# Optimization experiments

Measured on AMD Instinct MI355X. Metric: run time of the kernel, lower is better.

Reference implementation:

```python
import jax, jax.numpy as jnp
import numpy as np

N_NODES = 100000
N_EDGES = 1600000
NODE_DIM = 128
HIDDEN = 128
OUT_DIM = 128
N_GRAPHS = 64
LN_EPS = 1e-5


def setup_inputs() -> dict:
    key = jax.random.key(0)
    ks = jax.random.split(key, 14)

    def lin(k, fan_in, fan_out):
        bound = 1.0 / np.sqrt(fan_in)
        kw, kb = jax.random.split(k)
        W = jax.random.uniform(kw, (fan_in, fan_out), jnp.float32, -bound, bound)
        b = jax.random.uniform(kb, (fan_out,), jnp.float32, -bound, bound)
        return W, b

    node_features = jax.random.normal(ks[0], (N_NODES, NODE_DIM), jnp.float32)
    edge_index = jax.random.randint(ks[1], (2, N_EDGES), 0, N_NODES, jnp.int32)
    batch = jnp.sort(jax.random.randint(ks[2], (N_NODES,), 0, N_GRAPHS, jnp.int32))

    W1, b1 = lin(ks[3], NODE_DIM, HIDDEN)
    W2, b2 = lin(ks[4], HIDDEN, HIDDEN)
    W3, b3 = lin(ks[5], HIDDEN, OUT_DIM)
    Wm1, bm1 = lin(ks[6], OUT_DIM, HIDDEN)
    Wm2, bm2 = lin(ks[7], HIDDEN, OUT_DIM)
    ln_g = jnp.ones((OUT_DIM,), jnp.float32)
    ln_b = jnp.zeros((OUT_DIM,), jnp.float32)

    return dict(node_features=node_features, edge_index=edge_index, batch=batch,
                W1=W1, b1=b1, W2=W2, b2=b2, W3=W3, b3=b3,
                Wm1=Wm1, bm1=bm1, Wm2=Wm2, bm2=bm2, ln_g=ln_g, ln_b=ln_b)


def _gcn_precompute(edge_index, n_nodes):
    # Add self-loops; symmetric degree normalization (PyG GCNConv semantics).
    loops = jnp.arange(n_nodes, dtype=edge_index.dtype)
    src = jnp.concatenate([edge_index[0], loops])
    dst = jnp.concatenate([edge_index[1], loops])
    deg = jax.ops.segment_sum(jnp.ones_like(dst, jnp.float32), dst, num_segments=n_nodes)
    dinv = jax.lax.rsqrt(deg)  # deg >= 1 thanks to self-loops
    norm = dinv[src] * dinv[dst]  # [E + N]
    return src, dst, norm


def _gcn_layer(x, W, b, src, dst, norm, n_nodes):
    xw = x @ W                              # [N, F_out]
    msg = norm[:, None] * xw[src]           # [E+N, F_out] gather
    agg = jax.ops.segment_sum(msg, dst, num_segments=n_nodes)  # scatter-add
    return agg + b


def reference(node_features, edge_index, batch,
              W1, b1, W2, b2, W3, b3, Wm1, bm1, Wm2, bm2, ln_g, ln_b):
    n_nodes = node_features.shape[0]
    src, dst, norm = _gcn_precompute(edge_index, n_nodes)

    x = jax.nn.relu(_gcn_layer(node_features, W1, b1, src, dst, norm, n_nodes))
    x = jax.nn.relu(_gcn_layer(x, W2, b2, src, dst, norm, n_nodes))
    x = _gcn_layer(x, W3, b3, src, dst, norm, n_nodes)  # no relu on last layer

    # global mean pool per graph
    sums = jax.ops.segment_sum(x, batch, num_segments=N_GRAPHS)
    cnts = jax.ops.segment_sum(jnp.ones((n_nodes,), x.dtype), batch, num_segments=N_GRAPHS)
    g = sums / jnp.maximum(cnts, 1.0)[:, None]  # [G, OUT_DIM]

    # global reasoner MLP + LayerNorm
    h = jax.nn.relu(g @ Wm1 + bm1)
    y = h @ Wm2 + bm2
    mu = jnp.mean(y, axis=-1, keepdims=True)
    var = jnp.var(y, axis=-1, keepdims=True)
    y = (y - mu) * jax.lax.rsqrt(var + LN_EPS) * ln_g + ln_b
    return y
```

## Files before the change

kernel.cpp:

```cpp
#include <hip/hip_runtime.h>

#define FDIM 128
#define LN_EPS 1e-5f
#define NBKT_SHIFT 8
#define BKT_NODES 256
#define MAXBKT 512
#define CAP_SHIFT 13
#define BKT_CAP 8192

typedef short bf16x8 __attribute__((ext_vector_type(8)));
typedef float f32x4 __attribute__((ext_vector_type(4)));
typedef float f32x2 __attribute__((ext_vector_type(2)));
typedef ushort u16x8 __attribute__((ext_vector_type(8)));
typedef unsigned long long u64;
typedef long long i64;

static __device__ __forceinline__ ushort f2bf(float f) {
    union { float f; unsigned u; } v; v.f = f;
    unsigned r = v.u + 0x7FFFu + ((v.u >> 16) & 1u);
    return (ushort)(r >> 16);
}
static __device__ __forceinline__ float bf2f(ushort h) {
    union { unsigned u; float f; } v; v.u = ((unsigned)h) << 16;
    return v.f;
}
static __device__ __forceinline__ unsigned char f2fp8(float f) {
    return (unsigned char)__builtin_amdgcn_cvt_pk_fp8_f32(f, f, 0u, false);
}
static __device__ __forceinline__ float fp8tof(unsigned char b) {
    f32x2 p = __builtin_amdgcn_cvt_pk_f32_fp8((unsigned)b, false);
    return p[0];
}
static __device__ __forceinline__ void fp8x8_add(uint2 w, f32x2* acc) {
    acc[0] += __builtin_amdgcn_cvt_pk_f32_fp8(w.x, false);
    acc[1] += __builtin_amdgcn_cvt_pk_f32_fp8(w.x, true);
    acc[2] += __builtin_amdgcn_cvt_pk_f32_fp8(w.y, false);
    acc[3] += __builtin_amdgcn_cvt_pk_f32_fp8(w.y, true);
}

typedef __attribute__((address_space(3))) unsigned char lds_uchar;
typedef const __attribute__((address_space(1))) unsigned char glob_uchar;
static __device__ __forceinline__ void gload16(const unsigned char* g, unsigned char* l) {
    __builtin_amdgcn_global_load_lds((glob_uchar*)g, (lds_uchar*)l, 16, 0, 0);
}


__launch_bounds__(256)
__global__ void k_bkt_scatter(const int* __restrict__ src, const int* __restrict__ dst,
                              int* __restrict__ bcur, unsigned* __restrict__ bktA,
                              int E, int nbkt) {
    __shared__ int h[2][MAXBKT], lbase[2][MAXBKT], lcur[2][MAXBKT];
    const int t = threadIdx.x;
    const int half = t >> 7;
    for (int i = t; i < 2 * MAXBKT; i += 256) ((int*)h)[i] = 0;
    __syncthreads();
    const int E4 = E >> 2;
    const int4* s4p = (const int4*)src;
    const int4* d4p = (const int4*)dst;
    int4 sv[4], dv[4]; bool ok[4];
#pragma unroll
    for (int r = 0; r < 4; r++) {
        int i4 = blockIdx.x * 1024 + r * 256 + t;
        ok[r] = (i4 < E4);
        if (ok[r]) {
            sv[r] = s4p[i4]; dv[r] = d4p[i4];
            atomicAdd(&h[half][dv[r].x >> NBKT_SHIFT], 1);
            atomicAdd(&h[half][dv[r].y >> NBKT_SHIFT], 1);
            atomicAdd(&h[half][dv[r].z >> NBKT_SHIFT], 1);
            atomicAdd(&h[half][dv[r].w >> NBKT_SHIFT], 1);
        }
    }
    __syncthreads();
    for (int i = t; i < 2 * nbkt; i += 256) {
        const int hh = (i >= nbkt) ? 1 : 0;
        const int b = hh ? (i - nbkt) : i;
        const int c = h[hh][b];
        lbase[hh][b] = c ? ((b << CAP_SHIFT) + atomicAdd(&bcur[b], c)) : 0;
        lcur[hh][b] = 0;
    }
    __syncthreads();
#pragma unroll
    for (int r = 0; r < 4; r++) {
        if (!ok[r]) continue;
        int ss[4] = {sv[r].x, sv[r].y, sv[r].z, sv[r].w};
        int dd[4] = {dv[r].x, dv[r].y, dv[r].z, dv[r].w};
#pragma unroll
        for (int j = 0; j < 4; j++) {
            int b = dd[j] >> NBKT_SHIFT;
            int p = atomicAdd(&lcur[half][b], 1);
            bktA[(size_t)lbase[half][b] + p] =
                ((unsigned)ss[j] << NBKT_SHIFT) | (unsigned)(dd[j] & (BKT_NODES - 1));
        }
    }
}


__launch_bounds__(512)
__global__ void k_build(const unsigned* __restrict__ bktA, const int* __restrict__ bcur,
                        int2* __restrict__ rowinfo, float* __restrict__ dinv,
                        int* __restrict__ csr_src, int N) {
    __shared__ int sorted[BKT_CAP];
    __shared__ int cnt[BKT_NODES];
    __shared__ int cur[BKT_NODES];
    __shared__ int wpart[4], wbase[4];
    const int t = threadIdx.x;
    const int b = blockIdx.x;
    const int nb = b << NBKT_SHIFT;
    if (t < BKT_NODES) cnt[t] = 0;
    __syncthreads();
    const int beg = b << CAP_SHIFT;
    const int tot = bcur[b];
    for (int i = t; i < tot; i += 512)
        atomicAdd(&cnt[bktA[beg + i] & (BKT_NODES - 1)], 1);
    __syncthreads();
    const int lane = t & 63, wv = t >> 6;
    int my = 0, x = 0;
    if (t < BKT_NODES) {
        my = cnt[t];
        x = my;
#pragma unroll
        for (int off = 1; off < 64; off <<= 1) {
            int y = __shfl_up(x, off, 64);
            if (lane >= off) x += y;
        }
        if (lane == 63) wpart[wv] = x;
    }
    __syncthreads();
    if (t == 0) {
        int s = 0;
        for (int w = 0; w < 4; w++) { int tmp = wpart[w]; wbase[w] = s; s += tmp; }
    }
    __syncthreads();
    if (t < BKT_NODES) {
        const int incl = x + wbase[wv];
        const int rbeg = incl - my;
        cur[t] = rbeg;
        const int n = nb + t;
        if (n < N) {
            rowinfo[n] = make_int2(beg + rbeg, my);
            dinv[n] = rsqrtf((float)(my + 1));
        }
    }
    __syncthreads();
    for (int i = t; i < tot; i += 512) {
        unsigned pr = bktA[beg + i];
        int d = pr & (BKT_NODES - 1);
        int p = atomicAdd(&cur[d], 1);
        sorted[p] = (int)(pr >> NBKT_SHIFT);
    }
    __syncthreads();
    for (int i = t; i < tot; i += 512)
        csr_src[beg + i] = sorted[i];
}


__global__ void k_prep_w(const float* __restrict__ Wa, const float* __restrict__ Wb,
                         const float* __restrict__ Wc, ushort* __restrict__ Wt_b,
                         unsigned char* __restrict__ Wt8, float* __restrict__ gsums,
                         int* __restrict__ bcur) {
    int idx = blockIdx.x * 256 + threadIdx.x;
    int layer = idx >> 14;
    int r = idx & 16383;
    int nn = r >> 7, kk = r & 127;
    if (layer == 0) {
        Wt_b[r] = f2bf(Wa[kk * 128 + nn]);
    } else {
        const float* W = (layer == 1) ? Wb : Wc;
        Wt8[(size_t)(layer - 1) * 16384 + r] = f2fp8(W[kk * 128 + nn]);
    }
    if (idx < 8192) gsums[idx] = 0.f;
    if (idx < MAXBKT) bcur[idx] = 0;
}


__launch_bounds__(256)
__global__ void k_gemm_f32(const float* __restrict__ X, const ushort* __restrict__ Wt,
                           const float* __restrict__ dinv, unsigned char* __restrict__ C,
                           int N) {
    __shared__ __align__(16) ushort As[128][136];
    __shared__ ushort Ws[128][136];
    const int t = threadIdx.x;
    const int row0 = blockIdx.x * 128;

#pragma unroll
    for (int i = 0; i < 8; i++) {
        int c = t + i * 256;
        int r = c >> 4, c8 = (c & 15) * 8;
        *(bf16x8*)&Ws[r][c8] = *(const bf16x8*)&Wt[r * 128 + c8];
    }
#pragma unroll
    for (int i = 0; i < 8; i++) {
        int c = t + i * 256;
        int r = c >> 4, c8 = (c & 15) * 8;
        int row = row0 + r;
        bf16x8 pk = {0, 0, 0, 0, 0, 0, 0, 0};
        if (row < N) {
            const float* sp = X + (size_t)row * FDIM + c8;
            float4 u0 = *(const float4*)(sp);
            float4 u1 = *(const float4*)(sp + 4);
            pk[0] = (short)f2bf(u0.x); pk[1] = (short)f2bf(u0.y);
            pk[2] = (short)f2bf(u0.z); pk[3] = (short)f2bf(u0.w);
            pk[4] = (short)f2bf(u1.x); pk[5] = (short)f2bf(u1.y);
            pk[6] = (short)f2bf(u1.z); pk[7] = (short)f2bf(u1.w);
        }
        *(bf16x8*)&As[r][c8] = pk;
    }
    __syncthreads();

    const int w = t >> 6, l = t & 63;
    const int m = l & 15, q = l >> 4;
    const int r0 = w * 32;

    bf16x8 a0[4], a1[4];
#pragma unroll
    for (int ks = 0; ks < 4; ks++) {
        a0[ks] = *(const bf16x8*)&As[r0 + m][ks * 32 + q * 8];
        a1[ks] = *(const bf16x8*)&As[r0 + 16 + m][ks * 32 + q * 8];
    }

    f32x4 acc0[8], acc1[8];
#pragma unroll
    for (int ct = 0; ct < 8; ct++) { acc0[ct] = {0, 0, 0, 0}; acc1[ct] = {0, 0, 0, 0}; }

#pragma unroll
    for (int ct = 0; ct < 8; ct++) {
#pragma unroll
        for (int ks = 0; ks < 4; ks++) {
            bf16x8 b = *(const bf16x8*)&Ws[ct * 16 + m][ks * 32 + q * 8];
            acc0[ct] = __builtin_amdgcn_mfma_f32_16x16x32_bf16(a0[ks], b, acc0[ct], 0, 0, 0);
            acc1[ct] = __builtin_amdgcn_mfma_f32_16x16x32_bf16(a1[ks], b, acc1[ct], 0, 0, 0);
        }
    }

    float dv0[4], dv1[4];
#pragma unroll
    for (int r = 0; r < 4; r++) {
        int row = row0 + r0 + q * 4 + r;
        dv0[r] = (row < N) ? dinv[row] : 0.f;
        dv1[r] = (row + 16 < N) ? dinv[row + 16] : 0.f;
    }

    __syncthreads();
    char* Ab = (char*)&As[0][0];
#pragma unroll
    for (int ct = 0; ct < 8; ct++) {
#pragma unroll
        for (int r = 0; r < 4; r++) {
            int rl = r0 + q * 4 + r;
            Ab[rl * 128 + ct * 16 + m] = (char)f2fp8(acc0[ct][r] * dv0[r]);
            Ab[(rl + 16) * 128 + ct * 16 + m] = (char)f2fp8(acc1[ct][r] * dv1[r]);
        }
    }
    __syncthreads();
    const uint4* As4 = (const uint4*)Ab;
#pragma unroll
    for (int i = 0; i < 4; i++) {
        int c = t + i * 256;
        int row = c >> 3;
        int col = (c & 7) * 16;
        int grow = row0 + row;
        if (grow < N) *(uint4*)&C[(size_t)grow * FDIM + col] = As4[c];
    }
}


__launch_bounds__(256)
__global__ void k_gemm_fp8(const unsigned char* __restrict__ X,
                           const unsigned char* __restrict__ W8,
                           const float* __restrict__ dinv, unsigned char* __restrict__ C,
                           int N) {
    __shared__ __align__(16) unsigned char As[128 * 128];
    __shared__ __align__(16) unsigned char Ws[128 * 128];
    const int t = threadIdx.x;
    const int w = t >> 6, l = t & 63;
    const int row0 = blockIdx.x * 128;

    {
        const int lrow = l >> 3;
        const int scol = ((l & 7) ^ lrow) << 4;
        const unsigned char* gx = X + (size_t)(row0 + w * 32 + lrow) * FDIM + scol;
        const unsigned char* gw = W8 + (size_t)(w * 32 + lrow) * FDIM + scol;
#pragma unroll
        for (int i = 0; i < 4; i++) {
            gload16(gx + (size_t)i * 8 * FDIM, &As[(w * 32 + i * 8) * FDIM]);
            gload16(gw + (size_t)i * 8 * FDIM, &Ws[(w * 32 + i * 8) * FDIM]);
        }
    }
    __syncthreads();

    const int m = l & 15, q = l >> 4;
    const int r0 = w * 32;
    const int xa = (m & 7) << 4;

    i64 a0[4], a1[4];
#pragma unroll
    for (int ks = 0; ks < 4; ks++) {
        a0[ks] = *(const i64*)&As[(r0 + m) * FDIM + ((ks * 32 + q * 8) ^ xa)];
        a1[ks] = *(const i64*)&As[(r0 + 16 + m) * FDIM + ((ks * 32 + q * 8) ^ xa)];
    }

    f32x4 acc0[8], acc1[8];
#pragma unroll
    for (int ct = 0; ct < 8; ct++) { acc0[ct] = {0, 0, 0, 0}; acc1[ct] = {0, 0, 0, 0}; }

#pragma unroll
    for (int ct = 0; ct < 8; ct++) {
#pragma unroll
        for (int ks = 0; ks < 4; ks++) {
            i64 b = *(const i64*)&Ws[(ct * 16 + m) * FDIM + ((ks * 32 + q * 8) ^ xa)];
            acc0[ct] = __builtin_amdgcn_mfma_f32_16x16x32_fp8_fp8(a0[ks], b, acc0[ct], 0, 0, 0);
            acc1[ct] = __builtin_amdgcn_mfma_f32_16x16x32_fp8_fp8(a1[ks], b, acc1[ct], 0, 0, 0);
        }
    }

    float dv0[4], dv1[4];
#pragma unroll
    for (int r = 0; r < 4; r++) {
        int row = row0 + r0 + q * 4 + r;
        dv0[r] = (row < N) ? dinv[row] : 0.f;
        dv1[r] = (row + 16 < N) ? dinv[row + 16] : 0.f;
    }

    __syncthreads();
    char* Ab = (char*)&As[0];
#pragma unroll
    for (int ct = 0; ct < 8; ct++) {
#pragma unroll
        for (int r = 0; r < 4; r++) {
            int rl = r0 + q * 4 + r;
            Ab[rl * 128 + ct * 16 + m] = (char)f2fp8(acc0[ct][r] * dv0[r]);
            Ab[(rl + 16) * 128 + ct * 16 + m] = (char)f2fp8(acc1[ct][r] * dv1[r]);
        }
    }
    __syncthreads();
    const uint4* As4 = (const uint4*)Ab;
#pragma unroll
    for (int i = 0; i < 4; i++) {
        int c = t + i * 256;
        int row = c >> 3;
        int col = (c & 7) * 16;
        int grow = row0 + row;
        if (grow < N) *(uint4*)&C[(size_t)grow * FDIM + col] = As4[c];
    }
}


__launch_bounds__(256)
__global__ void k_aggregate(const unsigned char* __restrict__ xs8,
                            const int2* __restrict__ rowinfo,
                            const int* __restrict__ csr_src, const float* __restrict__ dinv,
                            const float* __restrict__ bias, unsigned char* __restrict__ out,
                            int N, int do_relu) {
    const int n = (blockIdx.x << 2) + (threadIdx.x >> 6);
    if (n >= N) return;
    const int l = threadIdx.x & 63;
    const int fl = l & 15;
    const int grp = l >> 4;
    const unsigned foff = (unsigned)fl << 3;

    f32x2 acc[4] = {{0, 0}, {0, 0}, {0, 0}, {0, 0}};
    if (grp == 0) {
        uint2 sv = *(const uint2*)(xs8 + (((unsigned)n << 7) | foff));
        fp8x8_add(sv, acc);
    }

    const int2 ri = rowinfo[n];
    const int beg = ri.x;
    const int deg = ri.y;

    for (int base = 0; base < deg; base += 64) {
        const int m = min(64, deg - base);
        int idx = 0;
        if (l < m) idx = csr_src[(unsigned)(beg + base + l)];
        int j = grp;
        if (j < m) {
            int s0 = __shfl(idx, j, 64);
            uint2 v0 = *(const uint2*)(xs8 + (((unsigned)s0 << 7) | foff));
            int j2 = j + 4;
            if (j2 < m) {
                int s1 = __shfl(idx, j2, 64);
                uint2 v1 = *(const uint2*)(xs8 + (((unsigned)s1 << 7) | foff));
                for (j = j2 + 4; j < m; j += 4) {
                    int s2 = __shfl(idx, j, 64);
                    uint2 v2 = *(const uint2*)(xs8 + (((unsigned)s2 << 7) | foff));
                    fp8x8_add(v0, acc);
                    v0 = v1; v1 = v2;
                }
                fp8x8_add(v0, acc);
                fp8x8_add(v1, acc);
            } else {
                fp8x8_add(v0, acc);
            }
        }
    }

    float a[8] = {acc[0][0], acc[0][1], acc[1][0], acc[1][1],
                  acc[2][0], acc[2][1], acc[3][0], acc[3][1]};
#pragma unroll
    for (int k = 0; k < 8; k++) {
        a[k] += __shfl_xor(a[k], 16, 64);
        a[k] += __shfl_xor(a[k], 32, 64);
    }

    if (grp == 0) {
        const float d = dinv[n];
        const float4 b0 = ((const float4*)bias)[fl * 2];
        const float4 b1 = ((const float4*)bias)[fl * 2 + 1];
        const float bb[8] = {b0.x, b0.y, b0.z, b0.w, b1.x, b1.y, b1.z, b1.w};
        float v[8];
#pragma unroll
        for (int k = 0; k < 8; k++) {
            v[k] = d * a[k] + bb[k];
            if (do_relu) v[k] = fmaxf(v[k], 0.f);
        }
        uint2 o;
        unsigned d0 = __builtin_amdgcn_cvt_pk_fp8_f32(v[0], v[1], 0u, false);
        o.x = __builtin_amdgcn_cvt_pk_fp8_f32(v[2], v[3], d0, true);
        unsigned d1 = __builtin_amdgcn_cvt_pk_fp8_f32(v[4], v[5], 0u, false);
        o.y = __builtin_amdgcn_cvt_pk_fp8_f32(v[6], v[7], d1, true);
        ((uint2*)out)[(size_t)n * 16 + fl] = o;
    }
}


__launch_bounds__(256)
__global__ void k_pool(const unsigned char* __restrict__ x3, const int* __restrict__ batch,
                       float* __restrict__ sums, int N) {
    const int t = threadIdx.x;
    const int fq = t & 31;
    const int sub = t >> 5;
    const int n0 = blockIdx.x * 256 + sub * 32;
    if (n0 >= N) return;
    const int n1 = (n0 + 32 < N) ? n0 + 32 : N;

    f32x4 acc = {0.f, 0.f, 0.f, 0.f};
    int cur = batch[n0];
    for (int n = n0; n < n1; n++) {
        int g = batch[n];
        if (g != cur) {
            float* s = &sums[cur * FDIM + (fq << 2)];
            atomicAdd(s + 0, acc[0]); atomicAdd(s + 1, acc[1]);
            atomicAdd(s + 2, acc[2]); atomicAdd(s + 3, acc[3]);
            acc = (f32x4){0.f, 0.f, 0.f, 0.f};
            cur = g;
        }
        unsigned w = *(const unsigned*)(x3 + ((size_t)n << 7) + (fq << 2));
        f32x2 lo = __builtin_amdgcn_cvt_pk_f32_fp8(w, false);
        f32x2 hi = __builtin_amdgcn_cvt_pk_f32_fp8(w, true);
        acc[0] += lo[0]; acc[1] += lo[1]; acc[2] += hi[0]; acc[3] += hi[1];
    }
    float* s = &sums[cur * FDIM + (fq << 2)];
    atomicAdd(s + 0, acc[0]); atomicAdd(s + 1, acc[1]);
    atomicAdd(s + 2, acc[2]); atomicAdd(s + 3, acc[3]);
}


__launch_bounds__(128)
__global__ void k_final(const float* __restrict__ sums, const int* __restrict__ batch, int N,
                        const float* __restrict__ Wm1, const float* __restrict__ bm1,
                        const float* __restrict__ Wm2, const float* __restrict__ bm2,
                        const float* __restrict__ ln_g, const float* __restrict__ ln_b,
                        float* __restrict__ out) {
    const int g = blockIdx.x;
    const int t = threadIdx.x;

    int lo = 0, hi = N;
    while (lo < hi) { int mid = (lo + hi) >> 1; if (batch[mid] < g) lo = mid + 1; else hi = mid; }
    int lo2 = lo, hi2 = N;
    while (lo2 < hi2) { int mid = (lo2 + hi2) >> 1; if (batch[mid] < g + 1) lo2 = mid + 1; else hi2 = mid; }
    float cnt = (float)(lo2 - lo);

    float gl = sums[g * FDIM + t] / fmaxf(cnt, 1.0f);

    __shared__ float gbuf[FDIM];
    __shared__ float hbuf[FDIM];
    __shared__ float wsum[4];
    gbuf[t] = gl;
    __syncthreads();

    float h = bm1[t];
#pragma unroll 8
    for (int k = 0; k < FDIM; k++) h += gbuf[k] * Wm1[k * FDIM + t];
    h = fmaxf(h, 0.f);
    hbuf[t] = h;
    __syncthreads();

    float y = bm2[t];
#pragma unroll 8
    for (int k = 0; k < FDIM; k++) y += hbuf[k] * Wm2[k * FDIM + t];

    float s = y, s2 = y * y;
#pragma unroll
    for (int off = 32; off > 0; off >>= 1) {
        s += __shfl_down(s, off, 64);
        s2 += __shfl_down(s2, off, 64);
    }
    if ((t & 63) == 0) { wsum[t >> 6] = s; wsum[2 + (t >> 6)] = s2; }
    __syncthreads();
    float sum = wsum[0] + wsum[1];
    float sumsq = wsum[2] + wsum[3];
    float mu = sum * (1.0f / FDIM);
    float var = sumsq * (1.0f / FDIM) - mu * mu;
    float r = rsqrtf(var + LN_EPS);
    out[g * FDIM + t] = (y - mu) * r * ln_g[t] + ln_b[t];
}


extern "C" void kernel_launch(void* const* d_in, const int* in_sizes, int n_in,
                              void* d_out, int out_size, void* d_ws, size_t ws_size,
                              hipStream_t stream) {
    const float* x_in  = (const float*)d_in[0];
    const int*   eidx  = (const int*)d_in[1];
    const int*   batch = (const int*)d_in[2];
    const float* W1 = (const float*)d_in[3];
    const float* b1 = (const float*)d_in[4];
    const float* W2 = (const float*)d_in[5];
    const float* b2 = (const float*)d_in[6];
    const float* W3 = (const float*)d_in[7];
    const float* b3 = (const float*)d_in[8];
    const float* Wm1 = (const float*)d_in[9];
    const float* bm1 = (const float*)d_in[10];
    const float* Wm2 = (const float*)d_in[11];
    const float* bm2 = (const float*)d_in[12];
    const float* ln_g = (const float*)d_in[13];
    const float* ln_b = (const float*)d_in[14];
    float* out = (float*)d_out;

    const int N = in_sizes[0] / FDIM;
    const int E = in_sizes[1] / 2;
    const int G = out_size / FDIM;

    const int* src = eidx;
    const int* dst = eidx + E;

    const int nbkt = (N + BKT_NODES - 1) >> NBKT_SHIFT;

    char* p = (char*)d_ws;
    unsigned* bktA = (unsigned*)p;    p += (size_t)nbkt * BKT_CAP * 4;
    unsigned char* B0q = (unsigned char*)p; p += (size_t)N * FDIM;
    unsigned char* B1q = (unsigned char*)p; p += (size_t)N * FDIM;
    int* csr_src = (int*)p;           p += (size_t)nbkt * BKT_CAP * 4;
    int2* rowinfo = (int2*)p;         p += (size_t)N * 8;
    float* dinv = (float*)p;          p += (size_t)N * 4;
    ushort* Wt_b = (ushort*)p;        p += 16384 * 2;
    unsigned char* Wt8 = (unsigned char*)p; p += 2 * 16384;
    float* gsums = (float*)p;         p += (size_t)G * FDIM * 4;
    int* bcur = (int*)p;              p += MAXBKT * 4;

    const int TPB = 256;
    dim3 blk(TPB);
    dim3 gAgg((N + 3) / 4);
    dim3 gTile((N + 127) / 128);
    const int nEb = (E + 4095) / 4096;

    k_prep_w<<<dim3(192), blk, 0, stream>>>(W1, W2, W3, Wt_b, Wt8, gsums, bcur);
    k_bkt_scatter<<<dim3(nEb), blk, 0, stream>>>(src, dst, bcur, bktA, E, nbkt);
    k_build<<<dim3(nbkt), dim3(512), 0, stream>>>(bktA, bcur, rowinfo, dinv, csr_src, N);

    k_gemm_f32<<<gTile, blk, 0, stream>>>(x_in, Wt_b, dinv, B0q, N);
    k_aggregate<<<gAgg, blk, 0, stream>>>(B0q, rowinfo, csr_src, dinv, b1, B1q, N, 1);

    k_gemm_fp8<<<gTile, blk, 0, stream>>>(B1q, Wt8, dinv, B0q, N);
    k_aggregate<<<gAgg, blk, 0, stream>>>(B0q, rowinfo, csr_src, dinv, b2, B1q, N, 1);

    k_gemm_fp8<<<gTile, blk, 0, stream>>>(B1q, Wt8 + 16384, dinv, B0q, N);
    k_aggregate<<<gAgg, blk, 0, stream>>>(B0q, rowinfo, csr_src, dinv, b3, B1q, N, 0);

    k_pool<<<dim3((N + 255) / 256), blk, 0, stream>>>(B1q, batch, gsums, N);
    k_final<<<dim3(G), dim3(FDIM), 0, stream>>>(gsums, batch, N, Wm1, bm1, Wm2, bm2,
                                                ln_g, ln_b, out);
}
```

Before: 388.5 us.

## Pad CSR rows to multiples of eight with zero dummy node, deepen gather pipeline

Each node's CSR row is padded to a multiple of 8 entries, and the padding points at an extra zero row (index N) appended to both feature buffers. The aggregation loop can then drop its tail branches and keep four gathers in flight, unrolled by eight. The aggregate kernel also moves to 512-thread blocks covering 8 nodes, and the bf16 conversion in the first GEMM uses the packed hardware instruction. The cost is extra padded gather traffic on zero rows and a bit more workspace, and the rounding of the bf16 conversion may differ slightly from the previous software routine.

```diff
diff --git a/kernel.cpp b/kernel.cpp
--- a/kernel.cpp
+++ b/kernel.cpp
@@ -20,9 +20,10 @@
     unsigned r = v.u + 0x7FFFu + ((v.u >> 16) & 1u);
     return (ushort)(r >> 16);
 }
-static __device__ __forceinline__ float bf2f(ushort h) {
-    union { unsigned u; float f; } v; v.u = ((unsigned)h) << 16;
-    return v.f;
+static __device__ __forceinline__ unsigned cvt_pk_bf16(float lo, float hi) {
+    unsigned r;
+    asm("v_cvt_pk_bf16_f32 %0, %1, %2" : "=v"(r) : "v"(lo), "v"(hi));
+    return r;
 }
 static __device__ __forceinline__ unsigned char f2fp8(float f) {
     return (unsigned char)__builtin_amdgcn_cvt_pk_fp8_f32(f, f, 0u, false);
@@ -103,6 +104,7 @@
     __shared__ int cnt[BKT_NODES];
     __shared__ int cur[BKT_NODES];
     __shared__ int wpart[4], wbase[4];
+    __shared__ int stot;
     const int t = threadIdx.x;
     const int b = blockIdx.x;
     const int nb = b << NBKT_SHIFT;
@@ -114,10 +116,11 @@
         atomicAdd(&cnt[bktA[beg + i] & (BKT_NODES - 1)], 1);
     __syncthreads();
     const int lane = t & 63, wv = t >> 6;
-    int my = 0, x = 0;
+    int my = 0, pm = 0, x = 0;
     if (t < BKT_NODES) {
         my = cnt[t];
-        x = my;
+        pm = (my + 7) & ~7;
+        x = pm;
 #pragma unroll
         for (int off = 1; off < 64; off <<= 1) {
             int y = __shfl_up(x, off, 64);
@@ -133,13 +136,15 @@
     __syncthreads();
     if (t < BKT_NODES) {
         const int incl = x + wbase[wv];
-        const int rbeg = incl - my;
+        const int rbeg = incl - pm;
         cur[t] = rbeg;
         const int n = nb + t;
         if (n < N) {
-            rowinfo[n] = make_int2(beg + rbeg, my);
+            rowinfo[n] = make_int2(beg + rbeg, pm);
             dinv[n] = rsqrtf((float)(my + 1));
         }
+        for (int i = rbeg + my; i < rbeg + pm; i++) sorted[i] = N;
+        if (t == BKT_NODES - 1) stot = incl;
     }
     __syncthreads();
     for (int i = t; i < tot; i += 512) {
@@ -149,7 +154,8 @@
         sorted[p] = (int)(pr >> NBKT_SHIFT);
     }
     __syncthreads();
-    for (int i = t; i < tot; i += 512)
+    const int tp = stot;
+    for (int i = t; i < tp; i += 512)
         csr_src[beg + i] = sorted[i];
 }
 
@@ -157,7 +163,8 @@
 __global__ void k_prep_w(const float* __restrict__ Wa, const float* __restrict__ Wb,
                          const float* __restrict__ Wc, ushort* __restrict__ Wt_b,
                          unsigned char* __restrict__ Wt8, float* __restrict__ gsums,
-                         int* __restrict__ bcur) {
+                         int* __restrict__ bcur, unsigned char* __restrict__ B0q,
+                         unsigned char* __restrict__ B1q, int N) {
     int idx = blockIdx.x * 256 + threadIdx.x;
     int layer = idx >> 14;
     int r = idx & 16383;
@@ -170,6 +177,9 @@
     }
     if (idx < 8192) gsums[idx] = 0.f;
     if (idx < MAXBKT) bcur[idx] = 0;
+    uint4 z = {0, 0, 0, 0};
+    if (idx < 8) ((uint4*)(B0q + (size_t)N * FDIM))[idx] = z;
+    else if (idx < 16) ((uint4*)(B1q + (size_t)N * FDIM))[idx - 8] = z;
 }
 
 
@@ -198,10 +208,12 @@
             const float* sp = X + (size_t)row * FDIM + c8;
             float4 u0 = *(const float4*)(sp);
             float4 u1 = *(const float4*)(sp + 4);
-            pk[0] = (short)f2bf(u0.x); pk[1] = (short)f2bf(u0.y);
-            pk[2] = (short)f2bf(u0.z); pk[3] = (short)f2bf(u0.w);
-            pk[4] = (short)f2bf(u1.x); pk[5] = (short)f2bf(u1.y);
-            pk[6] = (short)f2bf(u1.z); pk[7] = (short)f2bf(u1.w);
+            union { unsigned u[4]; bf16x8 v; } cv;
+            cv.u[0] = cvt_pk_bf16(u0.x, u0.y);
+            cv.u[1] = cvt_pk_bf16(u0.z, u0.w);
+            cv.u[2] = cvt_pk_bf16(u1.x, u1.y);
+            cv.u[3] = cvt_pk_bf16(u1.z, u1.w);
+            pk = cv.v;
         }
         *(bf16x8*)&As[r][c8] = pk;
     }
@@ -345,13 +357,13 @@
 }
 
 
-__launch_bounds__(256)
+__launch_bounds__(512)
 __global__ void k_aggregate(const unsigned char* __restrict__ xs8,
                             const int2* __restrict__ rowinfo,
                             const int* __restrict__ csr_src, const float* __restrict__ dinv,
                             const float* __restrict__ bias, unsigned char* __restrict__ out,
                             int N, int do_relu) {
-    const int n = (blockIdx.x << 2) + (threadIdx.x >> 6);
+    const int n = (blockIdx.x << 3) + (threadIdx.x >> 6);
     if (n >= N) return;
     const int l = threadIdx.x & 63;
     const int fl = l & 15;
@@ -372,25 +384,28 @@
         const int m = min(64, deg - base);
         int idx = 0;
         if (l < m) idx = csr_src[(unsigned)(beg + base + l)];
-        int j = grp;
-        if (j < m) {
-            int s0 = __shfl(idx, j, 64);
-            uint2 v0 = *(const uint2*)(xs8 + (((unsigned)s0 << 7) | foff));
-            int j2 = j + 4;
-            if (j2 < m) {
-                int s1 = __shfl(idx, j2, 64);
-                uint2 v1 = *(const uint2*)(xs8 + (((unsigned)s1 << 7) | foff));
-                for (j = j2 + 4; j < m; j += 4) {
-                    int s2 = __shfl(idx, j, 64);
-                    uint2 v2 = *(const uint2*)(xs8 + (((unsigned)s2 << 7) | foff));
-                    fp8x8_add(v0, acc);
-                    v0 = v1; v1 = v2;
-                }
+        int s0 = __shfl(idx, grp, 64);
+        uint2 v0 = *(const uint2*)(xs8 + (((unsigned)s0 << 7) | foff));
+        int s1 = __shfl(idx, grp + 4, 64);
+        uint2 v1 = *(const uint2*)(xs8 + (((unsigned)s1 << 7) | foff));
+        if (m >= 16) {
+            int s2 = __shfl(idx, grp + 8, 64);
+            uint2 v2 = *(const uint2*)(xs8 + (((unsigned)s2 << 7) | foff));
+            int s3 = __shfl(idx, grp + 12, 64);
+            uint2 v3 = *(const uint2*)(xs8 + (((unsigned)s3 << 7) | foff));
+            for (int j = grp + 16; j + 8 <= m + grp; j += 8) {
+                int sa = __shfl(idx, j, 64);
+                int sb = __shfl(idx, j + 4, 64);
                 fp8x8_add(v0, acc);
+                uint2 va = *(const uint2*)(xs8 + (((unsigned)sa << 7) | foff));
                 fp8x8_add(v1, acc);
-            } else {
-                fp8x8_add(v0, acc);
+                uint2 vb = *(const uint2*)(xs8 + (((unsigned)sb << 7) | foff));
+                v0 = v2; v1 = v3; v2 = va; v3 = vb;
             }
+            fp8x8_add(v0, acc); fp8x8_add(v1, acc);
+            fp8x8_add(v2, acc); fp8x8_add(v3, acc);
+        } else {
+            fp8x8_add(v0, acc); fp8x8_add(v1, acc);
         }
     }
 
@@ -537,8 +552,8 @@
 
     char* p = (char*)d_ws;
     unsigned* bktA = (unsigned*)p;    p += (size_t)nbkt * BKT_CAP * 4;
-    unsigned char* B0q = (unsigned char*)p; p += (size_t)N * FDIM;
-    unsigned char* B1q = (unsigned char*)p; p += (size_t)N * FDIM;
+    unsigned char* B0q = (unsigned char*)p; p += (size_t)(N + 1) * FDIM;
+    unsigned char* B1q = (unsigned char*)p; p += (size_t)(N + 1) * FDIM;
     int* csr_src = (int*)p;           p += (size_t)nbkt * BKT_CAP * 4;
     int2* rowinfo = (int2*)p;         p += (size_t)N * 8;
     float* dinv = (float*)p;          p += (size_t)N * 4;
@@ -549,22 +564,22 @@
 
     const int TPB = 256;
     dim3 blk(TPB);
-    dim3 gAgg((N + 3) / 4);
+    dim3 gAgg((N + 7) / 8);
     dim3 gTile((N + 127) / 128);
     const int nEb = (E + 4095) / 4096;
 
-    k_prep_w<<<dim3(192), blk, 0, stream>>>(W1, W2, W3, Wt_b, Wt8, gsums, bcur);
+    k_prep_w<<<dim3(192), blk, 0, stream>>>(W1, W2, W3, Wt_b, Wt8, gsums, bcur, B0q, B1q, N);
     k_bkt_scatter<<<dim3(nEb), blk, 0, stream>>>(src, dst, bcur, bktA, E, nbkt);
     k_build<<<dim3(nbkt), dim3(512), 0, stream>>>(bktA, bcur, rowinfo, dinv, csr_src, N);
 
     k_gemm_f32<<<gTile, blk, 0, stream>>>(x_in, Wt_b, dinv, B0q, N);
-    k_aggregate<<<gAgg, blk, 0, stream>>>(B0q, rowinfo, csr_src, dinv, b1, B1q, N, 1);
+    k_aggregate<<<gAgg, dim3(512), 0, stream>>>(B0q, rowinfo, csr_src, dinv, b1, B1q, N, 1);
 
     k_gemm_fp8<<<gTile, blk, 0, stream>>>(B1q, Wt8, dinv, B0q, N);
-    k_aggregate<<<gAgg, blk, 0, stream>>>(B0q, rowinfo, csr_src, dinv, b2, B1q, N, 1);
+    k_aggregate<<<gAgg, dim3(512), 0, stream>>>(B0q, rowinfo, csr_src, dinv, b2, B1q, N, 1);
 
     k_gemm_fp8<<<gTile, blk, 0, stream>>>(B1q, Wt8 + 16384, dinv, B0q, N);
-    k_aggregate<<<gAgg, blk, 0, stream>>>(B0q, rowinfo, csr_src, dinv, b3, B1q, N, 0);
+    k_aggregate<<<gAgg, dim3(512), 0, stream>>>(B0q, rowinfo, csr_src, dinv, b3, B1q, N, 0);
 
     k_pool<<<dim3((N + 255) / 256), blk, 0, stream>>>(B1q, batch, gsums, N);
     k_final<<<dim3(G), dim3(FDIM), 0, stream>>>(gsums, batch, N, Wm1, bm1, Wm2, bm2,
```

Result: faster. 378.0 us (-2.7%).
